# Optimization experiments

Measured on AMD Instinct MI355X. Metric: run time of the kernel, lower is better.

## Reference

```python
import jax, jax.numpy as jnp
import numpy as np

EPS = 1e-5

def _layernorm(h, g, b):
    mu = jnp.mean(h, axis=-1, keepdims=True)
    var = jnp.mean((h - mu) ** 2, axis=-1, keepdims=True)
    return (h - mu) / jnp.sqrt(var + EPS) * g + b

def _linoss_scan_im(A, dt, Bu):
    # A, dt: (N,) real; Bu: (B, L, N) complex64.
    # IM discretization of z' = -A x + B u, x' = z (LinOSS paper Eq. 3-4),
    # computed with a 2x2 block-diagonal associative (parallel) scan.
    S = 1.0 / (1.0 + dt * dt * A)  # Schur complement
    m11 = 1.0 - dt * dt * A * S
    m12 = -dt * A * S
    m21 = dt * S
    m22 = S
    fz = (m11 * dt) * Bu
    fx = (m21 * dt) * Bu
    Bt, L, N = Bu.shape
    br = lambda m: jnp.broadcast_to(m.astype(Bu.dtype), (Bt, L, N))
    elems = (br(m11), br(m12), br(m21), br(m22), fz, fx)

    def binop(ei, ej):
        a11i, a12i, a21i, a22i, bzi, bxi = ei
        a11j, a12j, a21j, a22j, bzj, bxj = ej
        return (a11j * a11i + a12j * a21i,
                a11j * a12i + a12j * a22i,
                a21j * a11i + a22j * a21i,
                a21j * a12i + a22j * a22i,
                a11j * bzi + a12j * bxi + bzj,
                a21j * bzi + a22j * bxi + bxj)

    res = jax.lax.associative_scan(binop, elems, axis=1)
    return res[5]  # x-component of the state, (B, L, N) complex

def setup_inputs():
    key = jax.random.key(0)
    ks = jax.random.split(key, 20)
    B, L, H_in, D_mod = 8, 2048, 128, 512
    s_in = np.float32(1.0 / np.sqrt(H_in))
    s_d = np.float32(1.0 / np.sqrt(D_mod))
    f32 = jnp.float32
    return {
        "x": jax.random.normal(ks[0], (B, L, H_in), f32),
        "W_in": jax.random.normal(ks[1], (D_mod, H_in), f32) * s_in,
        "b_in": jnp.zeros((D_mod,), f32),
        "W_enc": jax.random.normal(ks[2], (D_mod, D_mod), f32) * s_d,
        "b_enc": jnp.zeros((D_mod,), f32),
        "ln_g": jnp.ones((D_mod,), f32),
        "ln_b": jnp.zeros((D_mod,), f32),
        "A_diag": jax.random.uniform(ks[3], (D_mod,), f32),
        "log_steps": jax.random.normal(ks[4], (D_mod,), f32) * 0.5,
        "B_re": jax.random.normal(ks[5], (D_mod, D_mod), f32) * s_d,
        "B_im": jax.random.normal(ks[6], (D_mod, D_mod), f32) * s_d,
        "C_re": jax.random.normal(ks[7], (D_mod, D_mod), f32) * s_d,
        "C_im": jax.random.normal(ks[8], (D_mod, D_mod), f32) * s_d,
        "D": jax.random.normal(ks[9], (D_mod,), f32),
        "glu_w1": jax.random.normal(ks[10], (D_mod, D_mod), f32) * s_d,
        "glu_b1": jnp.zeros((D_mod,), f32),
        "glu_w2": jax.random.normal(ks[11], (D_mod, D_mod), f32) * s_d,
        "glu_b2": jnp.zeros((D_mod,), f32),
        "W_dec": jax.random.normal(ks[12], (D_mod, D_mod), f32) * s_d,
        "b_dec": jnp.zeros((D_mod,), f32),
        "W_out": jax.random.normal(ks[13], (H_in, D_mod), f32) * s_d,
        "b_out": jnp.zeros((H_in,), f32),
    }

def reference(x, W_in, b_in, W_enc, b_enc, ln_g, ln_b, A_diag, log_steps,
              B_re, B_im, C_re, C_im, D, glu_w1, glu_b1, glu_w2, glu_b2,
              W_dec, b_dec, W_out, b_out):
    h = x @ W_in.T + b_in                       # outer in_proj: (B, L, d)
    h = h @ W_enc.T + b_enc                     # LinOSS encoder
    skip = h
    hn = _layernorm(h, ln_g, ln_b)
    A = jax.nn.relu(A_diag)                     # nonnegative oscillator freqs
    dt = jax.nn.sigmoid(log_steps)              # per-state timestep in (0,1)
    Bc = (B_re + 1j * B_im).astype(jnp.complex64)
    Cc = (C_re + 1j * C_im).astype(jnp.complex64)
    Bu = jnp.einsum('blh,nh->bln', hn.astype(jnp.complex64), Bc)
    xs = _linoss_scan_im(A, dt, Bu)             # (B, L, N) complex
    y = jnp.einsum('bln,hn->blh', xs, Cc).real + D * hn
    y = jax.nn.gelu(y)
    y = (y @ glu_w1.T + glu_b1) * jax.nn.sigmoid(y @ glu_w2.T + glu_b2)  # GLU
    h = skip + y                                # residual (dropout = eval mode)
    h = h @ W_dec.T + b_dec                     # LinOSS decoder
    return h @ W_out.T + b_out                  # outer out_proj: (B, L, out)
```

## Files before the change

kernel.cpp:

```cpp
#include <hip/hip_runtime.h>
#include <cstddef>
#include <cstdint>
#include <math.h>

typedef _Float16 f16;
typedef f16 f16x8 __attribute__((ext_vector_type(8)));
typedef f16 f16x4 __attribute__((ext_vector_type(4)));
typedef float f32x4 __attribute__((ext_vector_type(4)));

constexpr int Bb   = 8;
constexpr int Ll   = 2048;
constexpr int Hin  = 128;
constexpr int Dm   = 512;
constexpr int Mrows = Bb * Ll;
constexpr int NC   = 32;
constexpr int CL   = Ll / NC;
constexpr int SZ1  = Bb * NC * Dm;

constexpr int TILE_ELE = 128 * 64;

static __device__ __forceinline__ float sigmoid_f(float x) {
    return 1.f / (1.f + expf(-x));
}
static __device__ __forceinline__ float gelu_tanh_f(float x) {
    float x3 = x * x * x;
    float t  = tanhf(0.7978845608028654f * (x + 0.044715f * x3));
    return 0.5f * x * (1.f + t);
}

static __device__ __forceinline__ void gld16(const f16* g, f16* l) {
    __builtin_amdgcn_global_load_lds(
        (const __attribute__((address_space(1))) void*)g,
        (__attribute__((address_space(3))) void*)l, 16, 0, 0);
}

struct CvtJob { const float* s; f16* d; int n; };
struct CvtJobs { CvtJob j[11]; };

__global__ __launch_bounds__(256) void convert_k(CvtJobs jobs) {
    const CvtJob jb = jobs.j[blockIdx.y];
    const int i = (blockIdx.x * 256 + threadIdx.x) * 4;
    if (i >= jb.n) return;
    const float4 v = *(const float4*)(jb.s + i);
    f16x4 o;
    o.x = (f16)v.x; o.y = (f16)v.y; o.z = (f16)v.z; o.w = (f16)v.w;
    *(f16x4*)(jb.d + i) = o;
}

template <int KM, int OUTF16>
__global__ __launch_bounds__(256) void gemm_mfma(
    const f16* __restrict__ A, const f16* __restrict__ A2,
    const f16* __restrict__ W, const f16* __restrict__ W2,
    const float* __restrict__ bias, const float* __restrict__ bias2,
    const f16* __restrict__ EX, const float* __restrict__ DV,
    void* __restrict__ Cout, void* __restrict__ Cout2, int M, int N, int K)
{
    constexpr int NTILE = (KM == 1) ? 4 : (KM == 0 ? 2 : 3);
    __shared__ f16 smem[NTILE * TILE_ELE];
    f16* As  = smem;
    f16* As2 = (KM == 1) ? smem + TILE_ELE : nullptr;
    f16* Bs  = smem + ((KM == 1) ? 2 : 1) * TILE_ELE;
    f16* Bs2 = (KM >= 1) ? Bs + TILE_ELE : nullptr;

    const int tid = threadIdx.x;
    const int l   = tid & 63;
    const int wid = tid >> 6;
    const int wr  = wid >> 1;
    const int wc  = wid & 1;
    const int lc  = l & 15;
    const int lr  = l >> 4;
    const int row0 = blockIdx.x * 128;
    const int col0 = blockIdx.y * 128;

    const int swz  = (l & 7) << 4;
    const int off0 = (((lr * 16)      ^ swz) >> 1);
    const int off1 = (((64 + lr * 16) ^ swz) >> 1);

    f32x4 acc[4][4];
    f32x4 acc2[(KM >= 2) ? 4 : 1][(KM >= 2) ? 4 : 1];
#pragma unroll
    for (int i = 0; i < 4; ++i)
#pragma unroll
        for (int j = 0; j < 4; ++j) {
            acc[i][j] = (f32x4){0.f, 0.f, 0.f, 0.f};
            if (KM >= 2) acc2[i][j] = (f32x4){0.f, 0.f, 0.f, 0.f};
        }

#define STAGE(LDS, GSRC)                                                     \
    {                                                                        \
        _Pragma("unroll")                                                    \
        for (int c = 0; c < 4; ++c) {                                        \
            const int chunk = c * 256 + tid;                                 \
            const int row   = chunk >> 3;                                    \
            const int kb    = ((chunk & 7) << 4) ^ ((row & 7) << 4);         \
            gld16(GSRC + (size_t)row * K + (kb >> 1), LDS + chunk * 8);      \
        }                                                                    \
    }

    for (int k0 = 0; k0 < K; k0 += 64) {
        __syncthreads();
        STAGE(As, A + (size_t)row0 * K + k0);
        STAGE(Bs, W + (size_t)col0 * K + k0);
        if (KM == 1) STAGE(As2, A2 + (size_t)row0 * K + k0);
        if (KM >= 1) STAGE(Bs2, W2 + (size_t)col0 * K + k0);
        __syncthreads();

#pragma unroll
        for (int ks = 0; ks < 2; ++ks) {
            const int off = ks ? off1 : off0;
            f16x8 aF[4], bF[4];
#pragma unroll
            for (int mi = 0; mi < 4; ++mi)
                aF[mi] = *(const f16x8*)(As + (wr * 64 + mi * 16 + lc) * 64 + off);
#pragma unroll
            for (int ni = 0; ni < 4; ++ni)
                bF[ni] = *(const f16x8*)(Bs + (wc * 64 + ni * 16 + lc) * 64 + off);
#pragma unroll
            for (int mi = 0; mi < 4; ++mi)
#pragma unroll
                for (int ni = 0; ni < 4; ++ni)
                    acc[mi][ni] = __builtin_amdgcn_mfma_f32_16x16x32_f16(
                        aF[mi], bF[ni], acc[mi][ni], 0, 0, 0);

            if (KM == 1) {
                f16x8 a2F[4], b2F[4];
#pragma unroll
                for (int mi = 0; mi < 4; ++mi)
                    a2F[mi] = *(const f16x8*)(As2 + (wr * 64 + mi * 16 + lc) * 64 + off);
#pragma unroll
                for (int ni = 0; ni < 4; ++ni)
                    b2F[ni] = *(const f16x8*)(Bs2 + (wc * 64 + ni * 16 + lc) * 64 + off);
#pragma unroll
                for (int mi = 0; mi < 4; ++mi)
#pragma unroll
                    for (int ni = 0; ni < 4; ++ni)
                        acc[mi][ni] = __builtin_amdgcn_mfma_f32_16x16x32_f16(
                            a2F[mi], b2F[ni], acc[mi][ni], 0, 0, 0);
            }
            if (KM >= 2) {
                f16x8 b2F[4];
#pragma unroll
                for (int ni = 0; ni < 4; ++ni)
                    b2F[ni] = *(const f16x8*)(Bs2 + (wc * 64 + ni * 16 + lc) * 64 + off);
#pragma unroll
                for (int mi = 0; mi < 4; ++mi)
#pragma unroll
                    for (int ni = 0; ni < 4; ++ni)
                        acc2[mi][ni] = __builtin_amdgcn_mfma_f32_16x16x32_f16(
                            aF[mi], b2F[ni], acc2[mi][ni], 0, 0, 0);
            }
        }
    }
#undef STAGE

    float* Cf32  = (float*)Cout;
    f16*   Cf16  = (f16*)Cout;
    float* C2f32 = (float*)Cout2;
#pragma unroll
    for (int mi = 0; mi < 4; ++mi) {
#pragma unroll
        for (int ni = 0; ni < 4; ++ni) {
            const int col   = col0 + wc * 64 + ni * 16 + lc;
            const int rbase = row0 + wr * 64 + mi * 16 + lr * 4;
            const f32x4 v = acc[mi][ni];
            if (KM == 0) {
                const float bv = bias ? bias[col] : 0.f;
#pragma unroll
                for (int r = 0; r < 4; ++r) {
                    const float o = v[r] + bv;
                    const size_t idx = (size_t)(rbase + r) * N + col;
                    if (OUTF16) Cf16[idx] = (f16)o; else Cf32[idx] = o;
                }
            } else if (KM == 1) {
                const float dv = DV[col];
#pragma unroll
                for (int r = 0; r < 4; ++r) {
                    const size_t idx = (size_t)(rbase + r) * N + col;
                    const float o = gelu_tanh_f(v[r] + dv * (float)EX[idx]);
                    if (OUTF16) Cf16[idx] = (f16)o; else Cf32[idx] = o;
                }
            } else if (KM == 2) {
                const float b1 = bias[col], b2 = bias2[col];
                const f32x4 v2 = acc2[mi][ni];
#pragma unroll
                for (int r = 0; r < 4; ++r) {
                    const size_t idx = (size_t)(rbase + r) * N + col;
                    const float o = (float)EX[idx] + (v[r] + b1) * sigmoid_f(v2[r] + b2);
                    if (OUTF16) Cf16[idx] = (f16)o; else Cf32[idx] = o;
                }
            } else {
                const f32x4 v2 = acc2[mi][ni];
#pragma unroll
                for (int r = 0; r < 4; ++r) {
                    const size_t idx = (size_t)(rbase + r) * N + col;
                    Cf32[idx]  = v[r];
                    C2f32[idx] = v2[r];
                }
            }
        }
    }
}

__global__ __launch_bounds__(256) void layernorm_f16(
    const f16* __restrict__ X, const float* __restrict__ g,
    const float* __restrict__ b, f16* __restrict__ Y)
{
    const int lane = threadIdx.x & 63;
    const int w    = threadIdx.x >> 6;
    const int row  = blockIdx.x * 4 + w;
    const size_t base = (size_t)row * Dm + lane * 8;

    const f16x8 v = *(const f16x8*)(X + base);
    float x[8];
    float s = 0.f, q = 0.f;
#pragma unroll
    for (int i = 0; i < 8; ++i) {
        x[i] = (float)v[i];
        s += x[i]; q += x[i] * x[i];
    }
#pragma unroll
    for (int off = 32; off > 0; off >>= 1) {
        s += __shfl_xor(s, off);
        q += __shfl_xor(q, off);
    }
    const float mu  = s * (1.f / 512.f);
    const float var = q * (1.f / 512.f) - mu * mu;
    const float rs  = rsqrtf(var + 1e-5f);

    const float4 g0 = *(const float4*)(g + lane * 8);
    const float4 g1 = *(const float4*)(g + lane * 8 + 4);
    const float4 b0 = *(const float4*)(b + lane * 8);
    const float4 b1 = *(const float4*)(b + lane * 8 + 4);
    const float gg[8] = {g0.x, g0.y, g0.z, g0.w, g1.x, g1.y, g1.z, g1.w};
    const float bb[8] = {b0.x, b0.y, b0.z, b0.w, b1.x, b1.y, b1.z, b1.w};
    f16x8 o;
#pragma unroll
    for (int i = 0; i < 8; ++i)
        o[i] = (f16)((x[i] - mu) * rs * gg[i] + bb[i]);
    *(f16x8*)(Y + base) = o;
}

__global__ void consts_k(const float* __restrict__ A_diag,
                         const float* __restrict__ log_steps,
                         float* __restrict__ cst)
{
    const int n = threadIdx.x;
    const float a   = fmaxf(A_diag[n], 0.f);
    const float dt  = 1.f / (1.f + expf(-log_steps[n]));
    const float d2a = dt * dt * a;
    const float S   = 1.f / (1.f + d2a);
    const float m11 = 1.f - d2a * S;
    const float m12 = -dt * a * S;
    const float m21 = dt * S;
    const float m22 = S;
    cst[n]            = m11;
    cst[Dm + n]       = m12;
    cst[2 * Dm + n]   = m21;
    cst[3 * Dm + n]   = m22;
    cst[4 * Dm + n]   = m11 * dt;
    cst[5 * Dm + n]   = m21 * dt;
}

__global__ __launch_bounds__(512) void scan_phase1(
    const float* __restrict__ bur, const float* __restrict__ bui,
    const float* __restrict__ cst, float* __restrict__ S1)
{
    const int n = threadIdx.x;
    const int c = blockIdx.x & (NC - 1);
    const int b = blockIdx.x >> 5;
    const float m11 = cst[n],          m12 = cst[Dm + n];
    const float m21 = cst[2 * Dm + n], m22 = cst[3 * Dm + n];
    const float c1  = cst[4 * Dm + n], c2  = cst[5 * Dm + n];

    float zr = 0.f, xr = 0.f, zi = 0.f, xi = 0.f;
    const size_t base = ((size_t)b * Ll + (size_t)c * CL) * Dm + n;
#pragma unroll 4
    for (int t = 0; t < CL; ++t) {
        const float br = bur[base + (size_t)t * Dm];
        const float bi = bui[base + (size_t)t * Dm];
        const float zrn = fmaf(m11, zr, fmaf(m12, xr, c1 * br));
        const float xrn = fmaf(m21, zr, fmaf(m22, xr, c2 * br));
        const float zin = fmaf(m11, zi, fmaf(m12, xi, c1 * bi));
        const float xin = fmaf(m21, zi, fmaf(m22, xi, c2 * bi));
        zr = zrn; xr = xrn; zi = zin; xi = xin;
    }
    const int idx = blockIdx.x * Dm + n;
    S1[idx]            = zr;
    S1[SZ1 + idx]      = xr;
    S1[2 * SZ1 + idx]  = zi;
    S1[3 * SZ1 + idx]  = xi;
}

__global__ __launch_bounds__(256) void scan_phase2(
    const float* __restrict__ S1, const float* __restrict__ cst,
    float* __restrict__ G)
{
    const int gidx = blockIdx.x * 256 + threadIdx.x;
    const int n = gidx & (Dm - 1);
    const int b = gidx >> 9;
    const float m11 = cst[n],          m12 = cst[Dm + n];
    const float m21 = cst[2 * Dm + n], m22 = cst[3 * Dm + n];

    float p11 = 1.f, p12 = 0.f, p21 = 0.f, p22 = 1.f;
    for (int i = 0; i < CL; ++i) {
        const float q11 = m11 * p11 + m12 * p21;
        const float q12 = m11 * p12 + m12 * p22;
        const float q21 = m21 * p11 + m22 * p21;
        const float q22 = m21 * p12 + m22 * p22;
        p11 = q11; p12 = q12; p21 = q21; p22 = q22;
    }

    float gzr = 0.f, gxr = 0.f, gzi = 0.f, gxi = 0.f;
    for (int c = 0; c < NC; ++c) {
        const int idx = (b * NC + c) * Dm + n;
        G[idx]           = gzr;
        G[SZ1 + idx]     = gxr;
        G[2 * SZ1 + idx] = gzi;
        G[3 * SZ1 + idx] = gxi;
        const float szr = S1[idx],           sxr = S1[SZ1 + idx];
        const float szi = S1[2 * SZ1 + idx], sxi = S1[3 * SZ1 + idx];
        const float t1 = p11 * gzr + p12 * gxr + szr;
        const float t2 = p21 * gzr + p22 * gxr + sxr;
        const float t3 = p11 * gzi + p12 * gxi + szi;
        const float t4 = p21 * gzi + p22 * gxi + sxi;
        gzr = t1; gxr = t2; gzi = t3; gxi = t4;
    }
}

__global__ __launch_bounds__(512) void scan_phase3(
    const float* __restrict__ bur, const float* __restrict__ bui,
    const float* __restrict__ cst, const float* __restrict__ G,
    f16* __restrict__ xrf, f16* __restrict__ xif)
{
    const int n = threadIdx.x;
    const int c = blockIdx.x & (NC - 1);
    const int b = blockIdx.x >> 5;
    const float m11 = cst[n],          m12 = cst[Dm + n];
    const float m21 = cst[2 * Dm + n], m22 = cst[3 * Dm + n];
    const float c1  = cst[4 * Dm + n], c2  = cst[5 * Dm + n];

    const int sidx = blockIdx.x * Dm + n;
    float zr = G[sidx];
    float xr = G[SZ1 + sidx];
    float zi = G[2 * SZ1 + sidx];
    float xi = G[3 * SZ1 + sidx];

    const size_t base = ((size_t)b * Ll + (size_t)c * CL) * Dm + n;
#pragma unroll 4
    for (int t = 0; t < CL; ++t) {
        const float br = bur[base + (size_t)t * Dm];
        const float bi = bui[base + (size_t)t * Dm];
        const float zrn = fmaf(m11, zr, fmaf(m12, xr, c1 * br));
        const float xrn = fmaf(m21, zr, fmaf(m22, xr, c2 * br));
        const float zin = fmaf(m11, zi, fmaf(m12, xi, c1 * bi));
        const float xin = fmaf(m21, zi, fmaf(m22, xi, c2 * bi));
        zr = zrn; xr = xrn; zi = zin; xi = xin;
        xrf[base + (size_t)t * Dm] = (f16)xr;
        xif[base + (size_t)t * Dm] = (f16)(-xi);
    }
}

extern "C" void kernel_launch(void* const* d_in, const int* in_sizes, int n_in,
                              void* d_out, int out_size, void* d_ws, size_t ws_size,
                              hipStream_t stream)
{
    const float* x         = (const float*)d_in[0];
    const float* W_in      = (const float*)d_in[1];
    const float* b_in      = (const float*)d_in[2];
    const float* W_enc     = (const float*)d_in[3];
    const float* b_enc     = (const float*)d_in[4];
    const float* ln_g      = (const float*)d_in[5];
    const float* ln_b      = (const float*)d_in[6];
    const float* A_diag    = (const float*)d_in[7];
    const float* log_steps = (const float*)d_in[8];
    const float* B_re      = (const float*)d_in[9];
    const float* B_im      = (const float*)d_in[10];
    const float* C_re      = (const float*)d_in[11];
    const float* C_im      = (const float*)d_in[12];
    const float* Dv        = (const float*)d_in[13];
    const float* glu_w1    = (const float*)d_in[14];
    const float* glu_b1    = (const float*)d_in[15];
    const float* glu_w2    = (const float*)d_in[16];
    const float* glu_b2    = (const float*)d_in[17];
    const float* W_dec     = (const float*)d_in[18];
    const float* b_dec     = (const float*)d_in[19];
    const float* W_out     = (const float*)d_in[20];
    const float* b_out     = (const float*)d_in[21];

    char* ws = (char*)d_ws;
    const size_t MB = 1 << 20;
    f16*   F0  = (f16*)(ws);
    f16*   F1  = (f16*)(ws + 16 * MB);
    f16*   F2  = (f16*)(ws + 32 * MB);
    f16*   F3  = (f16*)(ws + 48 * MB);
    float* BuR = (float*)(ws + 64 * MB);
    float* BuI = (float*)(ws + 96 * MB);
    f16*   GF  = (f16*)(ws + 64 * MB);
    f16*   XF  = (f16*)(ws + 128 * MB);
    float* S1  = (float*)(ws + 132 * MB);
    float* G   = (float*)(ws + 134 * MB);
    float* cst = (float*)(ws + 136 * MB);
    f16*   wbuf = (f16*)(ws + 137 * MB);
    f16* WFIN  = wbuf;
    f16* WFENC = WFIN  + 65536;
    f16* BFRE  = WFENC + 262144;
    f16* BFIM  = BFRE  + 262144;
    f16* CFRE  = BFIM  + 262144;
    f16* CFIM  = CFRE  + 262144;
    f16* W1F   = CFIM  + 262144;
    f16* W2F   = W1F   + 262144;
    f16* WFDEC = W2F   + 262144;
    f16* WFOUT = WFDEC + 262144;

    CvtJobs jobs;
    jobs.j[0]  = {x,      XF,    Mrows * Hin};
    jobs.j[1]  = {W_in,   WFIN,  Dm * Hin};
    jobs.j[2]  = {W_enc,  WFENC, Dm * Dm};
    jobs.j[3]  = {B_re,   BFRE,  Dm * Dm};
    jobs.j[4]  = {B_im,   BFIM,  Dm * Dm};
    jobs.j[5]  = {C_re,   CFRE,  Dm * Dm};
    jobs.j[6]  = {C_im,   CFIM,  Dm * Dm};
    jobs.j[7]  = {glu_w1, W1F,   Dm * Dm};
    jobs.j[8]  = {glu_w2, W2F,   Dm * Dm};
    jobs.j[9]  = {W_dec,  WFDEC, Dm * Dm};
    jobs.j[10] = {W_out,  WFOUT, Hin * Dm};

    convert_k<<<dim3((Mrows * Hin) / 1024, 11), 256, 0, stream>>>(jobs);
    consts_k<<<1, Dm, 0, stream>>>(A_diag, log_steps, cst);

    dim3 blk(256);
    dim3 g512(Mrows / 128, Dm / 128);
    dim3 g128(Mrows / 128, Hin / 128);

    gemm_mfma<0, 1><<<g512, blk, 0, stream>>>(XF, nullptr, WFIN, nullptr, b_in, nullptr,
                                              nullptr, nullptr, F0, nullptr, Mrows, Dm, Hin);
    gemm_mfma<0, 1><<<g512, blk, 0, stream>>>(F0, nullptr, WFENC, nullptr, b_enc, nullptr,
                                              nullptr, nullptr, F2, nullptr, Mrows, Dm, Dm);
    layernorm_f16<<<Mrows / 4, 256, 0, stream>>>(F2, ln_g, ln_b, F3);
    gemm_mfma<3, 0><<<g512, blk, 0, stream>>>(F3, nullptr, BFRE, BFIM, nullptr, nullptr,
                                              nullptr, nullptr, BuR, BuI, Mrows, Dm, Dm);
    scan_phase1<<<Bb * NC, 512, 0, stream>>>(BuR, BuI, cst, S1);
    scan_phase2<<<(Bb * Dm) / 256, 256, 0, stream>>>(S1, cst, G);
    scan_phase3<<<Bb * NC, 512, 0, stream>>>(BuR, BuI, cst, G, F0, F1);
    gemm_mfma<1, 1><<<g512, blk, 0, stream>>>(F0, F1, CFRE, CFIM, nullptr, nullptr,
                                              F3, Dv, GF, nullptr, Mrows, Dm, Dm);
    gemm_mfma<2, 1><<<g512, blk, 0, stream>>>(GF, nullptr, W1F, W2F, glu_b1, glu_b2,
                                              F2, nullptr, F3, nullptr, Mrows, Dm, Dm);
    gemm_mfma<0, 1><<<g512, blk, 0, stream>>>(F3, nullptr, WFDEC, nullptr, b_dec, nullptr,
                                              nullptr, nullptr, F2, nullptr, Mrows, Dm, Dm);
    gemm_mfma<0, 0><<<g128, blk, 0, stream>>>(F2, nullptr, WFOUT, nullptr, b_out, nullptr,
                                              nullptr, nullptr, (float*)d_out, nullptr, Mrows, Hin, Dm);
}
```

Before: 328.1 us.

## Fold adjacent linear layers, double-buffer GEMM LDS, and store Bu in fp16

Folds W_enc·W_in and W_out·W_dec into single weight matrices, computed on device, which removes two full 512-wide GEMMs from the activation path. The GEMM kernel is rewritten with double-buffered LDS staging so the next tile's loads overlap the current tile's MFMAs. The complex B projection and the GLU are split into separate single-output GEMMs. Bu is now stored as fp16 instead of fp32, cutting scan memory traffic at some precision cost. The product-weight kernels are naive serial loops and add launches, and splitting the GEMMs rereads the activations.

```diff
diff --git a/kernel.cpp b/kernel.cpp
--- a/kernel.cpp
+++ b/kernel.cpp
@@ -34,8 +34,44 @@
         (__attribute__((address_space(3))) void*)l, 16, 0, 0);
 }
 
+__global__ __launch_bounds__(128) void fuse_wc1(
+    const float* __restrict__ Wenc, const float* __restrict__ Win,
+    const float* __restrict__ b_in, const float* __restrict__ b_enc,
+    f16* __restrict__ Wc1, float* __restrict__ bc1)
+{
+    const int d2 = blockIdx.x;
+    const int t  = threadIdx.x;
+    float acc = 0.f;
+    for (int d = 0; d < Dm; ++d)
+        acc = fmaf(Wenc[d2 * Dm + d], Win[d * Hin + t], acc);
+    Wc1[d2 * Hin + t] = (f16)acc;
+    if (t == 0) {
+        float s = 0.f;
+        for (int d = 0; d < Dm; ++d) s = fmaf(Wenc[d2 * Dm + d], b_in[d], s);
+        bc1[d2] = s + b_enc[d2];
+    }
+}
+
+__global__ __launch_bounds__(512) void fuse_wc2(
+    const float* __restrict__ Wout, const float* __restrict__ Wdec,
+    const float* __restrict__ b_dec, const float* __restrict__ b_out,
+    f16* __restrict__ Wc2, float* __restrict__ bc2)
+{
+    const int o = blockIdx.x;
+    const int t = threadIdx.x;
+    float acc = 0.f;
+    for (int d = 0; d < Dm; ++d)
+        acc = fmaf(Wout[o * Dm + d], Wdec[d * Dm + t], acc);
+    Wc2[o * Dm + t] = (f16)acc;
+    if (t == 0) {
+        float s = 0.f;
+        for (int d = 0; d < Dm; ++d) s = fmaf(Wout[o * Dm + d], b_dec[d], s);
+        bc2[o] = s + b_out[o];
+    }
+}
+
 struct CvtJob { const float* s; f16* d; int n; };
-struct CvtJobs { CvtJob j[11]; };
+struct CvtJobs { CvtJob j[7]; };
 
 __global__ __launch_bounds__(256) void convert_k(CvtJobs jobs) {
     const CvtJob jb = jobs.j[blockIdx.y];
@@ -51,16 +87,12 @@
 __global__ __launch_bounds__(256) void gemm_mfma(
     const f16* __restrict__ A, const f16* __restrict__ A2,
     const f16* __restrict__ W, const f16* __restrict__ W2,
-    const float* __restrict__ bias, const float* __restrict__ bias2,
-    const f16* __restrict__ EX, const float* __restrict__ DV,
-    void* __restrict__ Cout, void* __restrict__ Cout2, int M, int N, int K)
-{
-    constexpr int NTILE = (KM == 1) ? 4 : (KM == 0 ? 2 : 3);
-    __shared__ f16 smem[NTILE * TILE_ELE];
-    f16* As  = smem;
-    f16* As2 = (KM == 1) ? smem + TILE_ELE : nullptr;
-    f16* Bs  = smem + ((KM == 1) ? 2 : 1) * TILE_ELE;
-    f16* Bs2 = (KM >= 1) ? Bs + TILE_ELE : nullptr;
+    const float* __restrict__ bias,
+    const f16* __restrict__ EX, const f16* __restrict__ EX2,
+    const float* __restrict__ DV,
+    void* __restrict__ Cout, int M, int N, int K)
+{
+    __shared__ f16 smem[4 * TILE_ELE];
 
     const int tid = threadIdx.x;
     const int l   = tid & 63;
@@ -72,90 +104,76 @@
     const int row0 = blockIdx.x * 128;
     const int col0 = blockIdx.y * 128;
 
+    const int Kst = (KM == 1) ? Dm : K;
+    const int KL  = (KM == 1) ? 2 * Dm : K;
+    const int NT  = KL >> 6;
+
     const int swz  = (l & 7) << 4;
-    const int off0 = (((lr * 16)      ^ swz) >> 1);
-    const int off1 = (((64 + lr * 16) ^ swz) >> 1);
+    const int off0 = ((lr * 16) ^ swz) >> 1;
+    const int off1 = ((64 + lr * 16) ^ swz) >> 1;
 
     f32x4 acc[4][4];
-    f32x4 acc2[(KM >= 2) ? 4 : 1][(KM >= 2) ? 4 : 1];
 #pragma unroll
     for (int i = 0; i < 4; ++i)
 #pragma unroll
-        for (int j = 0; j < 4; ++j) {
-            acc[i][j] = (f32x4){0.f, 0.f, 0.f, 0.f};
-            if (KM >= 2) acc2[i][j] = (f32x4){0.f, 0.f, 0.f, 0.f};
-        }
-
-#define STAGE(LDS, GSRC)                                                     \
+        for (int j = 0; j < 4; ++j) acc[i][j] = (f32x4){0.f, 0.f, 0.f, 0.f};
+
+    auto asrc = [&](int k0) -> const f16* {
+        if (KM == 1 && k0 >= Dm) return A2 + (size_t)row0 * Dm + (k0 - Dm);
+        return A + (size_t)row0 * Kst + k0;
+    };
+    auto wsrc = [&](int k0) -> const f16* {
+        if (KM == 1 && k0 >= Dm) return W2 + (size_t)col0 * Dm + (k0 - Dm);
+        return W + (size_t)col0 * Kst + k0;
+    };
+
+#define STAGE(DST, SRC)                                                      \
     {                                                                        \
         _Pragma("unroll")                                                    \
         for (int c = 0; c < 4; ++c) {                                        \
             const int chunk = c * 256 + tid;                                 \
             const int row   = chunk >> 3;                                    \
             const int kb    = ((chunk & 7) << 4) ^ ((row & 7) << 4);         \
-            gld16(GSRC + (size_t)row * K + (kb >> 1), LDS + chunk * 8);      \
+            gld16(SRC + (size_t)row * Kst + (kb >> 1), DST + chunk * 8);     \
         }                                                                    \
     }
 
-    for (int k0 = 0; k0 < K; k0 += 64) {
-        __syncthreads();
-        STAGE(As, A + (size_t)row0 * K + k0);
-        STAGE(Bs, W + (size_t)col0 * K + k0);
-        if (KM == 1) STAGE(As2, A2 + (size_t)row0 * K + k0);
-        if (KM >= 1) STAGE(Bs2, W2 + (size_t)col0 * K + k0);
-        __syncthreads();
-
+    STAGE(smem, asrc(0));
+    STAGE(smem + 2 * TILE_ELE, wsrc(0));
+    __syncthreads();
+
+    int cur = 0;
+    for (int kt = 0; kt < NT; ++kt) {
+        if (kt + 1 < NT) {
+            STAGE(smem + (cur ^ 1) * TILE_ELE, asrc((kt + 1) << 6));
+            STAGE(smem + (2 + (cur ^ 1)) * TILE_ELE, wsrc((kt + 1) << 6));
+        }
+        const f16* Asc = smem + cur * TILE_ELE;
+        const f16* Bsc = smem + (2 + cur) * TILE_ELE;
 #pragma unroll
         for (int ks = 0; ks < 2; ++ks) {
             const int off = ks ? off1 : off0;
             f16x8 aF[4], bF[4];
 #pragma unroll
             for (int mi = 0; mi < 4; ++mi)
-                aF[mi] = *(const f16x8*)(As + (wr * 64 + mi * 16 + lc) * 64 + off);
+                aF[mi] = *(const f16x8*)(Asc + (wr * 64 + mi * 16 + lc) * 64 + off);
 #pragma unroll
             for (int ni = 0; ni < 4; ++ni)
-                bF[ni] = *(const f16x8*)(Bs + (wc * 64 + ni * 16 + lc) * 64 + off);
+                bF[ni] = *(const f16x8*)(Bsc + (wc * 64 + ni * 16 + lc) * 64 + off);
 #pragma unroll
             for (int mi = 0; mi < 4; ++mi)
 #pragma unroll
                 for (int ni = 0; ni < 4; ++ni)
                     acc[mi][ni] = __builtin_amdgcn_mfma_f32_16x16x32_f16(
                         aF[mi], bF[ni], acc[mi][ni], 0, 0, 0);
-
-            if (KM == 1) {
-                f16x8 a2F[4], b2F[4];
-#pragma unroll
-                for (int mi = 0; mi < 4; ++mi)
-                    a2F[mi] = *(const f16x8*)(As2 + (wr * 64 + mi * 16 + lc) * 64 + off);
-#pragma unroll
-                for (int ni = 0; ni < 4; ++ni)
-                    b2F[ni] = *(const f16x8*)(Bs2 + (wc * 64 + ni * 16 + lc) * 64 + off);
-#pragma unroll
-                for (int mi = 0; mi < 4; ++mi)
-#pragma unroll
-                    for (int ni = 0; ni < 4; ++ni)
-                        acc[mi][ni] = __builtin_amdgcn_mfma_f32_16x16x32_f16(
-                            a2F[mi], b2F[ni], acc[mi][ni], 0, 0, 0);
-            }
-            if (KM >= 2) {
-                f16x8 b2F[4];
-#pragma unroll
-                for (int ni = 0; ni < 4; ++ni)
-                    b2F[ni] = *(const f16x8*)(Bs2 + (wc * 64 + ni * 16 + lc) * 64 + off);
-#pragma unroll
-                for (int mi = 0; mi < 4; ++mi)
-#pragma unroll
-                    for (int ni = 0; ni < 4; ++ni)
-                        acc2[mi][ni] = __builtin_amdgcn_mfma_f32_16x16x32_f16(
-                            aF[mi], b2F[ni], acc2[mi][ni], 0, 0, 0);
-            }
         }
+        __syncthreads();
+        cur ^= 1;
     }
 #undef STAGE
 
-    float* Cf32  = (float*)Cout;
-    f16*   Cf16  = (f16*)Cout;
-    float* C2f32 = (float*)Cout2;
+    float* Cf32 = (float*)Cout;
+    f16*   Cf16 = (f16*)Cout;
 #pragma unroll
     for (int mi = 0; mi < 4; ++mi) {
 #pragma unroll
@@ -179,22 +197,13 @@
                     const float o = gelu_tanh_f(v[r] + dv * (float)EX[idx]);
                     if (OUTF16) Cf16[idx] = (f16)o; else Cf32[idx] = o;
                 }
-            } else if (KM == 2) {
-                const float b1 = bias[col], b2 = bias2[col];
-                const f32x4 v2 = acc2[mi][ni];
+            } else {
+                const float bv = bias[col];
 #pragma unroll
                 for (int r = 0; r < 4; ++r) {
                     const size_t idx = (size_t)(rbase + r) * N + col;
-                    const float o = (float)EX[idx] + (v[r] + b1) * sigmoid_f(v2[r] + b2);
+                    const float o = (float)EX[idx] + (float)EX2[idx] * sigmoid_f(v[r] + bv);
                     if (OUTF16) Cf16[idx] = (f16)o; else Cf32[idx] = o;
-                }
-            } else {
-                const f32x4 v2 = acc2[mi][ni];
-#pragma unroll
-                for (int r = 0; r < 4; ++r) {
-                    const size_t idx = (size_t)(rbase + r) * N + col;
-                    Cf32[idx]  = v[r];
-                    C2f32[idx] = v2[r];
                 }
             }
         }
@@ -262,7 +271,7 @@
 }
 
 __global__ __launch_bounds__(512) void scan_phase1(
-    const float* __restrict__ bur, const float* __restrict__ bui,
+    const f16* __restrict__ bur, const f16* __restrict__ bui,
     const float* __restrict__ cst, float* __restrict__ S1)
 {
     const int n = threadIdx.x;
@@ -276,8 +285,8 @@
     const size_t base = ((size_t)b * Ll + (size_t)c * CL) * Dm + n;
 #pragma unroll 4
     for (int t = 0; t < CL; ++t) {
-        const float br = bur[base + (size_t)t * Dm];
-        const float bi = bui[base + (size_t)t * Dm];
+        const float br = (float)bur[base + (size_t)t * Dm];
+        const float bi = (float)bui[base + (size_t)t * Dm];
         const float zrn = fmaf(m11, zr, fmaf(m12, xr, c1 * br));
         const float xrn = fmaf(m21, zr, fmaf(m22, xr, c2 * br));
         const float zin = fmaf(m11, zi, fmaf(m12, xi, c1 * bi));
@@ -328,7 +337,7 @@
 }
 
 __global__ __launch_bounds__(512) void scan_phase3(
-    const float* __restrict__ bur, const float* __restrict__ bui,
+    const f16* __restrict__ bur, const f16* __restrict__ bui,
     const float* __restrict__ cst, const float* __restrict__ G,
     f16* __restrict__ xrf, f16* __restrict__ xif)
 {
@@ -348,8 +357,8 @@
     const size_t base = ((size_t)b * Ll + (size_t)c * CL) * Dm + n;
 #pragma unroll 4
     for (int t = 0; t < CL; ++t) {
-        const float br = bur[base + (size_t)t * Dm];
-        const float bi = bui[base + (size_t)t * Dm];
+        const float br = (float)bur[base + (size_t)t * Dm];
+        const float bi = (float)bui[base + (size_t)t * Dm];
         const float zrn = fmaf(m11, zr, fmaf(m12, xr, c1 * br));
         const float xrn = fmaf(m21, zr, fmaf(m22, xr, c2 * br));
         const float zin = fmaf(m11, zi, fmaf(m12, xi, c1 * bi));
@@ -389,65 +398,64 @@
 
     char* ws = (char*)d_ws;
     const size_t MB = 1 << 20;
-    f16*   F0  = (f16*)(ws);
-    f16*   F1  = (f16*)(ws + 16 * MB);
-    f16*   F2  = (f16*)(ws + 32 * MB);
-    f16*   F3  = (f16*)(ws + 48 * MB);
-    float* BuR = (float*)(ws + 64 * MB);
-    float* BuI = (float*)(ws + 96 * MB);
-    f16*   GF  = (f16*)(ws + 64 * MB);
-    f16*   XF  = (f16*)(ws + 128 * MB);
-    float* S1  = (float*)(ws + 132 * MB);
-    float* G   = (float*)(ws + 134 * MB);
-    float* cst = (float*)(ws + 136 * MB);
-    f16*   wbuf = (f16*)(ws + 137 * MB);
-    f16* WFIN  = wbuf;
-    f16* WFENC = WFIN  + 65536;
-    f16* BFRE  = WFENC + 262144;
-    f16* BFIM  = BFRE  + 262144;
-    f16* CFRE  = BFIM  + 262144;
-    f16* CFIM  = CFRE  + 262144;
-    f16* W1F   = CFIM  + 262144;
-    f16* W2F   = W1F   + 262144;
-    f16* WFDEC = W2F   + 262144;
-    f16* WFOUT = WFDEC + 262144;
+    f16*   F2   = (f16*)(ws);
+    f16*   F3   = (f16*)(ws + 16 * MB);
+    f16*   F0   = (f16*)(ws + 32 * MB);
+    f16*   F1   = (f16*)(ws + 48 * MB);
+    f16*   BuRh = (f16*)(ws + 64 * MB);
+    f16*   BuIh = (f16*)(ws + 80 * MB);
+    f16*   P1   = BuRh;
+    f16*   GF   = BuIh;
+    f16*   XF   = (f16*)(ws + 96 * MB);
+    float* S1   = (float*)(ws + 100 * MB);
+    float* G    = (float*)(ws + 102 * MB);
+    float* cst  = (float*)(ws + 104 * MB);
+    f16*   Wc1  = (f16*)(ws + 105 * MB);
+    f16*   Wc2  = (f16*)(ws + 106 * MB);
+    float* bc1  = (float*)(ws + 107 * MB);
+    float* bc2  = (float*)(ws + 107 * MB + 4096);
+    f16*   wbuf = (f16*)(ws + 108 * MB);
+    f16* BFRE = wbuf;
+    f16* BFIM = BFRE + 262144;
+    f16* CFRE = BFIM + 262144;
+    f16* CFIM = CFRE + 262144;
+    f16* W1F  = CFIM + 262144;
+    f16* W2F  = W1F  + 262144;
 
     CvtJobs jobs;
-    jobs.j[0]  = {x,      XF,    Mrows * Hin};
-    jobs.j[1]  = {W_in,   WFIN,  Dm * Hin};
-    jobs.j[2]  = {W_enc,  WFENC, Dm * Dm};
-    jobs.j[3]  = {B_re,   BFRE,  Dm * Dm};
-    jobs.j[4]  = {B_im,   BFIM,  Dm * Dm};
-    jobs.j[5]  = {C_re,   CFRE,  Dm * Dm};
-    jobs.j[6]  = {C_im,   CFIM,  Dm * Dm};
-    jobs.j[7]  = {glu_w1, W1F,   Dm * Dm};
-    jobs.j[8]  = {glu_w2, W2F,   Dm * Dm};
-    jobs.j[9]  = {W_dec,  WFDEC, Dm * Dm};
-    jobs.j[10] = {W_out,  WFOUT, Hin * Dm};
-
-    convert_k<<<dim3((Mrows * Hin) / 1024, 11), 256, 0, stream>>>(jobs);
+    jobs.j[0] = {x,      XF,   Mrows * Hin};
+    jobs.j[1] = {B_re,   BFRE, Dm * Dm};
+    jobs.j[2] = {B_im,   BFIM, Dm * Dm};
+    jobs.j[3] = {C_re,   CFRE, Dm * Dm};
+    jobs.j[4] = {C_im,   CFIM, Dm * Dm};
+    jobs.j[5] = {glu_w1, W1F,  Dm * Dm};
+    jobs.j[6] = {glu_w2, W2F,  Dm * Dm};
+
+    convert_k<<<dim3((Mrows * Hin) / 1024, 7), 256, 0, stream>>>(jobs);
+    fuse_wc1<<<Dm, Hin, 0, stream>>>(W_enc, W_in, b_in, b_enc, Wc1, bc1);
+    fuse_wc2<<<Hin, Dm, 0, stream>>>(W_out, W_dec, b_dec, b_out, Wc2, bc2);
     consts_k<<<1, Dm, 0, stream>>>(A_diag, log_steps, cst);
 
     dim3 blk(256);
     dim3 g512(Mrows / 128, Dm / 128);
     dim3 g128(Mrows / 128, Hin / 128);
 
-    gemm_mfma<0, 1><<<g512, blk, 0, stream>>>(XF, nullptr, WFIN, nullptr, b_in, nullptr,
-                                              nullptr, nullptr, F0, nullptr, Mrows, Dm, Hin);
-    gemm_mfma<0, 1><<<g512, blk, 0, stream>>>(F0, nullptr, WFENC, nullptr, b_enc, nullptr,
-                                              nullptr, nullptr, F2, nullptr, Mrows, Dm, Dm);
+    gemm_mfma<0, 1><<<g512, blk, 0, stream>>>(XF, nullptr, Wc1, nullptr, bc1,
+                                              nullptr, nullptr, nullptr, F2, Mrows, Dm, Hin);
     layernorm_f16<<<Mrows / 4, 256, 0, stream>>>(F2, ln_g, ln_b, F3);
-    gemm_mfma<3, 0><<<g512, blk, 0, stream>>>(F3, nullptr, BFRE, BFIM, nullptr, nullptr,
-                                              nullptr, nullptr, BuR, BuI, Mrows, Dm, Dm);
-    scan_phase1<<<Bb * NC, 512, 0, stream>>>(BuR, BuI, cst, S1);
+    gemm_mfma<0, 1><<<g512, blk, 0, stream>>>(F3, nullptr, BFRE, nullptr, nullptr,
+                                              nullptr, nullptr, nullptr, BuRh, Mrows, Dm, Dm);
+    gemm_mfma<0, 1><<<g512, blk, 0, stream>>>(F3, nullptr, BFIM, nullptr, nullptr,
+                                              nullptr, nullptr, nullptr, BuIh, Mrows, Dm, Dm);
+    scan_phase1<<<Bb * NC, 512, 0, stream>>>(BuRh, BuIh, cst, S1);
     scan_phase2<<<(Bb * Dm) / 256, 256, 0, stream>>>(S1, cst, G);
-    scan_phase3<<<Bb * NC, 512, 0, stream>>>(BuR, BuI, cst, G, F0, F1);
-    gemm_mfma<1, 1><<<g512, blk, 0, stream>>>(F0, F1, CFRE, CFIM, nullptr, nullptr,
-                                              F3, Dv, GF, nullptr, Mrows, Dm, Dm);
-    gemm_mfma<2, 1><<<g512, blk, 0, stream>>>(GF, nullptr, W1F, W2F, glu_b1, glu_b2,
-                                              F2, nullptr, F3, nullptr, Mrows, Dm, Dm);
-    gemm_mfma<0, 1><<<g512, blk, 0, stream>>>(F3, nullptr, WFDEC, nullptr, b_dec, nullptr,
-                                              nullptr, nullptr, F2, nullptr, Mrows, Dm, Dm);
-    gemm_mfma<0, 0><<<g128, blk, 0, stream>>>(F2, nullptr, WFOUT, nullptr, b_out, nullptr,
-                                              nullptr, nullptr, (float*)d_out, nullptr, Mrows, Hin, Dm);
-}
+    scan_phase3<<<Bb * NC, 512, 0, stream>>>(BuRh, BuIh, cst, G, F0, F1);
+    gemm_mfma<1, 1><<<g512, blk, 0, stream>>>(F0, F1, CFRE, CFIM, nullptr,
+                                              F3, nullptr, Dv, GF, Mrows, Dm, Dm);
+    gemm_mfma<0, 1><<<g512, blk, 0, stream>>>(GF, nullptr, W1F, nullptr, glu_b1,
+                                              nullptr, nullptr, nullptr, P1, Mrows, Dm, Dm);
+    gemm_mfma<2, 1><<<g512, blk, 0, stream>>>(GF, nullptr, W2F, nullptr, glu_b2,
+                                              F2, P1, nullptr, F3, Mrows, Dm, Dm);
+    gemm_mfma<0, 0><<<g128, blk, 0, stream>>>(F3, nullptr, Wc2, nullptr, bc2,
+                                              nullptr, nullptr, nullptr, (float*)d_out, Mrows, Hin, Dm);
+}
```

New measurement: 332.1 us. Within noise of the previous version (+1.2%).
